# Kernel optimization log

Measured on AMD Instinct MI355X. Metric: run time of the kernel, lower is better.

Reference implementation:

```python
import jax, jax.numpy as jnp
import numpy as np

# Morphological dilation (max-plus "convolution"), per-channel:
#   out[b,y,x,c] = max_{i,j} ( x_padded[b, y+i, x+j, c] + w[i, j, c] )
# TF SAME padding for k=4, stride 1: pad_total=3 -> pad_before=1, pad_after=2.
# Out-of-bounds positions act as -inf (identity for max), matching tf.nn.dilation2d.

def setup_inputs() -> dict:
    key = jax.random.key(0)
    kx, kw = jax.random.split(key)
    x = jax.random.normal(kx, (8, 512, 512, 32), dtype=jnp.float32)
    w = jax.random.normal(kw, (4, 4, 32), dtype=jnp.float32) * 0.1
    return {"x": x, "w": w}


def reference(x, w):
    kh, kw_ = w.shape[0], w.shape[1]
    H, W = x.shape[1], x.shape[2]
    pt, pl = (kh - 1) // 2, (kw_ - 1) // 2          # pad before (TF SAME)
    pb, pr = kh - 1 - pt, kw_ - 1 - pl              # pad after
    xp = jnp.pad(x, ((0, 0), (pt, pb), (pl, pr), (0, 0)),
                 constant_values=-jnp.inf)
    out = jnp.full(x.shape, -jnp.inf, dtype=x.dtype)
    # Small fixed kh*kw loop (16 iters); each iter is a fused shift+add+max.
    for i in range(kh):
        for j in range(kw_):
            out = jnp.maximum(out, xp[:, i:i + H, j:j + W, :] + w[i, j])
    return out
```

## Files before the change

kernel.cpp:

```cpp
#include <hip/hip_runtime.h>
#include <math.h>


constexpr int H = 512;
constexpr int W = 512;
constexpr int C = 32;
constexpr int T = 16;

template<bool EDGE>
__device__ __forceinline__ void dil_body(const float* __restrict__ xb,
                                         const float wv[16],
                                         float acc[T],
                                         const int y0, const int xp) {
    const float NI = -INFINITY;
#pragma unroll
    for (int r = 0; r < T + 3; ++r) {
        int yy = y0 - 1 + r;
        bool yok = true;
        if (EDGE) {
            yok = ((unsigned)yy < (unsigned)H);
            yy = min(max(yy, 0), H - 1);
        }
        const float* rowp = xb + (size_t)yy * (W * C);

        float px[4];
#pragma unroll
        for (int j = 0; j < 4; ++j) {
            int xx = xp + j - 1;
            if (EDGE) {
                bool ok = yok & ((unsigned)xx < (unsigned)W);
                xx = min(max(xx, 0), W - 1);
                float v = rowp[(size_t)xx * C];
                px[j] = ok ? v : NI;
            } else {
                px[j] = rowp[(size_t)xx * C];
            }
        }

#pragma unroll
        for (int i = 0; i < 4; ++i) {
            const int t = r - i;
            if (t < 0 || t >= T) continue;
            float v = fmaxf(fmaxf(px[0] + wv[i * 4 + 0], px[1] + wv[i * 4 + 1]),
                            fmaxf(px[2] + wv[i * 4 + 2], px[3] + wv[i * 4 + 3]));
            acc[t] = fmaxf(acc[t], v);
        }
    }
}

__global__ __launch_bounds__(256)
void dil2d_kernel(const float* __restrict__ xin,
                  const float* __restrict__ wt,
                  float* __restrict__ out) {
    const int c  = threadIdx.x & (C - 1);
    const int xl = threadIdx.x >> 5;
    const int xp = blockIdx.x * 8 + xl;
    const int y0 = blockIdx.y * T;
    const int b  = blockIdx.z;

    float wv[16];
#pragma unroll
    for (int k = 0; k < 16; ++k)
        wv[k] = wt[k * C + c];

    float acc[T];
#pragma unroll
    for (int t = 0; t < T; ++t) acc[t] = -INFINITY;

    const float* xb = xin + (size_t)b * H * W * C + c;

    const bool yedge = (blockIdx.y == 0) || (blockIdx.y == gridDim.y - 1);
    const bool xedge = (blockIdx.x == 0) || (blockIdx.x == gridDim.x - 1);

    if (yedge | xedge) dil_body<true >(xb, wv, acc, y0, xp);
    else               dil_body<false>(xb, wv, acc, y0, xp);

    float* ob = out + (((size_t)b * H + y0) * W + xp) * C + c;
#pragma unroll
    for (int t = 0; t < T; ++t)
        __builtin_nontemporal_store(acc[t], ob + (size_t)t * W * C);
}

extern "C" void kernel_launch(void* const* d_in, const int* in_sizes, int n_in,
                              void* d_out, int out_size, void* d_ws, size_t ws_size,
                              hipStream_t stream) {
    const float* x = (const float*)d_in[0];
    const float* w = (const float*)d_in[1];
    float* o = (float*)d_out;

    dim3 block(256);
    dim3 grid(W / 8,
              H / T,
              8);
    dil2d_kernel<<<grid, block, 0, stream>>>(x, w, o);
}
```

Before: 97.36 us.

## Stream rows through a rotating 4-entry accumulator ring over 128-row chunks

Each thread now walks 128 output rows, keeping only a 4-slot rotating accumulator ring and storing each output row as soon as it completes. This replaces the 16-row tile with 3 halo rows, so the vertical halo re-read falls from 19/16 to 131/128 and register pressure drops. The cost is 4x fewer blocks (fewer waves to hide latency), a runtime loop instead of full unrolling, and per-row y bounds checks on every step.

```diff
diff --git a/kernel.cpp b/kernel.cpp
--- a/kernel.cpp
+++ b/kernel.cpp
@@ -5,46 +5,64 @@
 constexpr int H = 512;
 constexpr int W = 512;
 constexpr int C = 32;
-constexpr int T = 16;
+constexpr int CHUNK = 128;
 
-template<bool EDGE>
-__device__ __forceinline__ void dil_body(const float* __restrict__ xb,
-                                         const float wv[16],
-                                         float acc[T],
-                                         const int y0, const int xp) {
+template<int P, bool STORE, bool XEDGE>
+__device__ __forceinline__ void step(const float* __restrict__ xb,
+                                     float* __restrict__ ob,
+                                     const float wv[16], float acc[4],
+                                     const int yy, const int xp) {
+    constexpr int S0 = P;
+    constexpr int S1 = (P + 1) & 3;
+    constexpr int S2 = (P + 2) & 3;
+    constexpr int S3 = (P + 3) & 3;
     const float NI = -INFINITY;
+
+    const bool yok = ((unsigned)yy < (unsigned)H);
+    const int  yc  = min(max(yy, 0), H - 1);
+    const float* rowp = xb + (size_t)yc * (W * C);
+
+    float px[4];
 #pragma unroll
-    for (int r = 0; r < T + 3; ++r) {
-        int yy = y0 - 1 + r;
-        bool yok = true;
-        if (EDGE) {
-            yok = ((unsigned)yy < (unsigned)H);
-            yy = min(max(yy, 0), H - 1);
+    for (int j = 0; j < 4; ++j) {
+        int xx = xp + j - 1;
+        bool ok = yok;
+        if (XEDGE) {
+            ok = ok & ((unsigned)xx < (unsigned)W);
+            xx = min(max(xx, 0), W - 1);
         }
-        const float* rowp = xb + (size_t)yy * (W * C);
+        float v = rowp[(size_t)xx * C];
+        px[j] = ok ? v : NI;
+    }
 
-        float px[4];
-#pragma unroll
-        for (int j = 0; j < 4; ++j) {
-            int xx = xp + j - 1;
-            if (EDGE) {
-                bool ok = yok & ((unsigned)xx < (unsigned)W);
-                xx = min(max(xx, 0), W - 1);
-                float v = rowp[(size_t)xx * C];
-                px[j] = ok ? v : NI;
-            } else {
-                px[j] = rowp[(size_t)xx * C];
-            }
-        }
+    acc[S1] = fmaxf(acc[S1], fmaxf(fmaxf(px[0] + wv[ 0], px[1] + wv[ 1]),
+                                   fmaxf(px[2] + wv[ 2], px[3] + wv[ 3])));
+    acc[S0] = fmaxf(acc[S0], fmaxf(fmaxf(px[0] + wv[ 4], px[1] + wv[ 5]),
+                                   fmaxf(px[2] + wv[ 6], px[3] + wv[ 7])));
+    acc[S3] = fmaxf(acc[S3], fmaxf(fmaxf(px[0] + wv[ 8], px[1] + wv[ 9]),
+                                   fmaxf(px[2] + wv[10], px[3] + wv[11])));
+    acc[S2] = fmaxf(acc[S2], fmaxf(fmaxf(px[0] + wv[12], px[1] + wv[13]),
+                                   fmaxf(px[2] + wv[14], px[3] + wv[15])));
 
-#pragma unroll
-        for (int i = 0; i < 4; ++i) {
-            const int t = r - i;
-            if (t < 0 || t >= T) continue;
-            float v = fmaxf(fmaxf(px[0] + wv[i * 4 + 0], px[1] + wv[i * 4 + 1]),
-                            fmaxf(px[2] + wv[i * 4 + 2], px[3] + wv[i * 4 + 3]));
-            acc[t] = fmaxf(acc[t], v);
-        }
+    if (STORE)
+        __builtin_nontemporal_store(acc[S2], ob + (size_t)(yy - 2) * (W * C));
+    acc[S2] = NI;
+}
+
+template<bool XEDGE>
+__device__ __forceinline__ void chunk_body(const float* __restrict__ xb,
+                                           float* __restrict__ ob,
+                                           const float wv[16], float acc[4],
+                                           const int y0, const int xp) {
+    step<3, false, XEDGE>(xb, ob, wv, acc, y0 - 1, xp);
+    step<0, false, XEDGE>(xb, ob, wv, acc, y0,     xp);
+    step<1, false, XEDGE>(xb, ob, wv, acc, y0 + 1, xp);
+    for (int s = 0; s < CHUNK; s += 4) {
+        const int yy = y0 + 2 + s;
+        step<2, true, XEDGE>(xb, ob, wv, acc, yy,     xp);
+        step<3, true, XEDGE>(xb, ob, wv, acc, yy + 1, xp);
+        step<0, true, XEDGE>(xb, ob, wv, acc, yy + 2, xp);
+        step<1, true, XEDGE>(xb, ob, wv, acc, yy + 3, xp);
     }
 }
 
@@ -55,7 +73,7 @@
     const int c  = threadIdx.x & (C - 1);
     const int xl = threadIdx.x >> 5;
     const int xp = blockIdx.x * 8 + xl;
-    const int y0 = blockIdx.y * T;
+    const int y0 = blockIdx.y * CHUNK;
     const int b  = blockIdx.z;
 
     float wv[16];
@@ -63,22 +81,14 @@
     for (int k = 0; k < 16; ++k)
         wv[k] = wt[k * C + c];
 
-    float acc[T];
-#pragma unroll
-    for (int t = 0; t < T; ++t) acc[t] = -INFINITY;
+    float acc[4] = { -INFINITY, -INFINITY, -INFINITY, -INFINITY };
 
     const float* xb = xin + (size_t)b * H * W * C + c;
+    float* ob = out + ((size_t)b * H * W + xp) * C + c;
 
-    const bool yedge = (blockIdx.y == 0) || (blockIdx.y == gridDim.y - 1);
     const bool xedge = (blockIdx.x == 0) || (blockIdx.x == gridDim.x - 1);
-
-    if (yedge | xedge) dil_body<true >(xb, wv, acc, y0, xp);
-    else               dil_body<false>(xb, wv, acc, y0, xp);
-
-    float* ob = out + (((size_t)b * H + y0) * W + xp) * C + c;
-#pragma unroll
-    for (int t = 0; t < T; ++t)
-        __builtin_nontemporal_store(acc[t], ob + (size_t)t * W * C);
+    if (xedge) chunk_body<true >(xb, ob, wv, acc, y0, xp);
+    else       chunk_body<false>(xb, ob, wv, acc, y0, xp);
 }
 
 extern "C" void kernel_launch(void* const* d_in, const int* in_sizes, int n_in,
@@ -90,7 +100,7 @@
 
     dim3 block(256);
     dim3 grid(W / 8,
-              H / T,
+              H / CHUNK,
               8);
     dil2d_kernel<<<grid, block, 0, stream>>>(x, w, o);
 }
```

Result: slower. 103.1 us (+5.9%).
